# Performance work log

Measured on AMD Instinct MI355X. Metric: run time of the kernel, lower is better.

## Reference

```python
import jax, jax.numpy as jnp
import numpy as np

D = 2048          # in_features == out_features (d_model)
H_TOTAL = 8192    # hidden_features, split across experts
E = 8             # num_experts
K = 2             # num_selects (top-k)
HE = H_TOTAL // E # per-expert hidden size
B, S = 2, 2048


def setup_inputs() -> dict:
    key = jax.random.key(0)
    ks = jax.random.split(key, 8)
    scale_up = 1.0 / np.sqrt(D)
    scale_dn = 1.0 / np.sqrt(HE)
    return {
        "x": jax.random.normal(ks[0], (B, S, D), dtype=jnp.float32),
        # mlp gate network: Linear(D,E,no bias) -> tanh -> Linear(E,E,no bias)
        "Wg1": jax.random.normal(ks[1], (E, D), dtype=jnp.float32) * 0.02,
        "Wg2": jax.random.normal(ks[2], (E, E), dtype=jnp.float32) * 0.2,
        # per-expert GLU-MLP weights (stacked over expert axis)
        "Wup": jax.random.uniform(ks[3], (E, HE, D), dtype=jnp.float32, minval=-scale_up, maxval=scale_up),
        "bup": jax.random.uniform(ks[4], (E, HE), dtype=jnp.float32, minval=-scale_up, maxval=scale_up),
        "Wdown": jax.random.uniform(ks[5], (E, D, HE), dtype=jnp.float32, minval=-scale_dn, maxval=scale_dn),
        "bdown": jax.random.uniform(ks[6], (E, D), dtype=jnp.float32, minval=-scale_dn, maxval=scale_dn),
    }


def reference(x, Wg1, Wg2, Wup, bup, Wdown, bdown):
    Bd, Sd, Dd = x.shape
    T = Bd * Sd
    xt = x.reshape(T, Dd)                                   # [T, D] tokens

    # ---- TopKBalancedNoisyGate (eval mode: no noise) ----
    logits = jnp.tanh(xt @ Wg1.T) @ Wg2.T                   # [T, E]
    _, top_idx = jax.lax.top_k(logits, K)                   # [T, K]
    top_logits = jnp.take_along_axis(logits, top_idx, axis=1)
    top_scores = jax.nn.softmax(top_logits.astype(jnp.float32), axis=1).astype(logits.dtype)
    # scatter top-k scores into dense [T, E] (zeros elsewhere)
    rows = jnp.arange(T)[:, None]
    scores = jnp.zeros_like(logits).at[rows, top_idx].set(top_scores)

    # ---- per-expert Linear-GLU experts: up -> silu -> down, score-combined ----
    up = jnp.einsum('td,ehd->teh', xt, Wup) + bup           # [T, E, HE]
    h = jax.nn.silu(up)
    down = jnp.einsum('teh,eoh->teo', h, Wdown) + bdown     # [T, E, D]
    out = jnp.einsum('te,teo->to', scores, down)            # [T, D]
    return out.reshape(Bd, Sd, Dd)
```

## Files before the change

### kernel.cpp

```cpp
#include <hip/hip_runtime.h>
#include <hip/hip_bf16.h>

#define D_DIM 2048
#define HE_DIM 1024
#define E_NUM 8
#define T_NUM 4096
#define TK_NUM 8192
#define TILE 128
#define BK 64
#define MAXROWS 9216
#define MAXMT 72

#define M_CNT(e)  ((e) * 32)
#define M_FILL(e) (256 + (e) * 32)
#define M_OFF  512
#define M_NMT  520
#define M_TE   528
#define M_TB   600
#define M_TICKET 704
#define M_INTS 1024

typedef unsigned short u16;
typedef __attribute__((ext_vector_type(8))) short bf16x8;
typedef __attribute__((ext_vector_type(4))) float f32x4;

#define OFF_XB   ((size_t)0)
#define OFF_WUPB (OFF_XB + (size_t)T_NUM * D_DIM * 2)
#define OFF_SLOT ((size_t)0)
#define OFF_WDNB (OFF_WUPB + (size_t)E_NUM * HE_DIM * D_DIM * 2)
#define OFF_H    (OFF_WDNB + (size_t)E_NUM * D_DIM * HE_DIM * 2)
#define OFF_SCR  (OFF_H + (size_t)MAXROWS * HE_DIM * 2)
#define OFF_EIDX (OFF_SCR + (size_t)TK_NUM * 4)
#define OFF_RT   (OFF_EIDX + (size_t)TK_NUM * 4)
#define OFF_RS   (OFF_RT + (size_t)MAXROWS * 4)
#define OFF_META (OFF_RS + (size_t)MAXROWS * 4)

__device__ __forceinline__ u16 f2bf(float f) {
  unsigned u = __float_as_uint(f);
  u += 0x7FFFu + ((u >> 16) & 1u);
  return (u16)(u >> 16);
}
__device__ __forceinline__ float bf_lo(unsigned u) { return __uint_as_float(u << 16); }
__device__ __forceinline__ float bf_hi(unsigned u) { return __uint_as_float(u & 0xFFFF0000u); }

__device__ __forceinline__ void gload16(const void* g, void* l) {
  __builtin_amdgcn_global_load_lds((const __attribute__((address_space(1))) void*)g,
                                   (__attribute__((address_space(3))) void*)l,
                                   16, 0, 0);
}

__global__ void k_cvt2(const float4* __restrict__ s1, const float4* __restrict__ s2,
                       ushort4* __restrict__ d1, ushort4* __restrict__ d2, int n4,
                       int* __restrict__ meta, int* __restrict__ rows_slot,
                       float* __restrict__ rowscore) {
  const int i0 = blockIdx.x * blockDim.x + threadIdx.x;
  if (i0 < M_INTS) meta[i0] = 0;
  if (i0 < MAXROWS) { rows_slot[i0] = -1; rowscore[i0] = 0.0f; }
  const int st = gridDim.x * blockDim.x;
  for (int i = i0; i < 2 * n4; i += st) {
    const float4* s = (i < n4) ? s1 : s2;
    ushort4* d = (i < n4) ? d1 : d2;
    int j = (i < n4) ? i : i - n4;
    float4 v = s[j];
    ushort4 o;
    o.x = f2bf(v.x); o.y = f2bf(v.y); o.z = f2bf(v.z); o.w = f2bf(v.w);
    d[j] = o;
  }
}

__global__ __launch_bounds__(256) void k_gate(
    const float4* __restrict__ x4, const float4* __restrict__ Wg1_4,
    const float* __restrict__ Wg2, ushort4* __restrict__ xb4,
    int* __restrict__ eidx, float* __restrict__ scr, int* __restrict__ meta) {
  __shared__ float4 wg1s[E_NUM * (D_DIM / 4)];
  __shared__ int cnt_s[E_NUM];
  __shared__ int lastf;
  const int tid = threadIdx.x;
  if (tid < E_NUM) cnt_s[tid] = 0;
#pragma unroll
  for (int i = 0; i < 16; ++i) wg1s[tid + i * 256] = Wg1_4[tid + i * 256];
  __syncthreads();

  const int w = tid >> 6;
  const int lane = tid & 63;
  for (int j = 0; j < 4; ++j) {
    const int t = blockIdx.x * 16 + w * 4 + j;
    float acc[E_NUM];
#pragma unroll
    for (int e = 0; e < E_NUM; ++e) acc[e] = 0.f;
#pragma unroll
    for (int i = 0; i < 8; ++i) {
      const int c = lane + i * 64;
      float4 xv = x4[(size_t)t * 512 + c];
      ushort4 o;
      o.x = f2bf(xv.x); o.y = f2bf(xv.y); o.z = f2bf(xv.z); o.w = f2bf(xv.w);
      xb4[(size_t)t * 512 + c] = o;
#pragma unroll
      for (int e = 0; e < E_NUM; ++e) {
        float4 wv = wg1s[e * 512 + c];
        acc[e] += xv.x * wv.x + xv.y * wv.y + xv.z * wv.z + xv.w * wv.w;
      }
    }
#pragma unroll
    for (int e = 0; e < E_NUM; ++e) {
      float v = acc[e];
#pragma unroll
      for (int off = 32; off; off >>= 1) v += __shfl_xor(v, off, 64);
      acc[e] = v;
    }
    if (lane == 0) {
      float l1[E_NUM], lg[E_NUM];
#pragma unroll
      for (int e = 0; e < E_NUM; ++e) l1[e] = tanhf(acc[e]);
#pragma unroll
      for (int i = 0; i < E_NUM; ++i) {
        float s = 0.f;
#pragma unroll
        for (int e = 0; e < E_NUM; ++e) s += l1[e] * Wg2[i * E_NUM + e];
        lg[i] = s;
      }
      int i0 = 0; float v0 = lg[0];
#pragma unroll
      for (int i = 1; i < E_NUM; ++i) if (lg[i] > v0) { v0 = lg[i]; i0 = i; }
      int i1 = -1; float v1 = -3.4e38f;
#pragma unroll
      for (int i = 0; i < E_NUM; ++i) if (i != i0 && lg[i] > v1) { v1 = lg[i]; i1 = i; }
      float e1 = __expf(v1 - v0);
      float s0 = 1.f / (1.f + e1);
      float s1 = e1 * s0;
      eidx[t * 2] = i0; eidx[t * 2 + 1] = i1;
      scr[t * 2] = s0;  scr[t * 2 + 1] = s1;
      atomicAdd(&cnt_s[i0], 1);
      atomicAdd(&cnt_s[i1], 1);
    }
  }
  __syncthreads();
  if (tid < E_NUM) atomicAdd(&meta[M_CNT(tid)], cnt_s[tid]);

  if (tid == 0) {
    __threadfence();
    lastf = (atomicAdd(&meta[M_TICKET], 1) == (int)gridDim.x - 1);
  }
  __syncthreads();
  if (lastf && tid < 64) {
    const int l2 = tid;
    int cnt = (l2 < E_NUM) ? atomicAdd(&meta[M_CNT(l2)], 0) : 0;
    int tiles = (cnt + TILE - 1) / TILE;
    int pre = tiles;
#pragma unroll
    for (int off = 1; off < E_NUM; off <<= 1) {
      int v = __shfl_up(pre, off, 64);
      if (l2 >= off && l2 < E_NUM) pre += v;
    }
    int tb_excl = pre - tiles;
    if (l2 < E_NUM) meta[M_OFF + l2] = tb_excl * TILE;
    const int nmt = __shfl(pre, E_NUM - 1, 64);
    if (l2 == 0) meta[M_NMT] = nmt;
    int tb[E_NUM];
#pragma unroll
    for (int k = 0; k < E_NUM; ++k) tb[k] = __shfl(tb_excl, k, 64);
    for (int mt = l2; mt < nmt; mt += 64) {
      int e = 0;
#pragma unroll
      for (int k = 1; k < E_NUM; ++k) if (mt >= tb[k]) e = k;
      meta[M_TE + mt] = e;
      meta[M_TB + mt] = mt * TILE;
    }
  }
}

__global__ void k_assign(const int* __restrict__ eidx, const float* __restrict__ scr,
                         int* __restrict__ meta, int* __restrict__ rows_slot,
                         float* __restrict__ rowscore) {
  int i = blockIdx.x * blockDim.x + threadIdx.x;
  const int lane = threadIdx.x & 63;
  int e = eidx[i];
  int pos = 0;
#pragma unroll
  for (int ex = 0; ex < E_NUM; ++ex) {
    unsigned long long m = __ballot(e == ex);
    if (e == ex) {
      int leader = __ffsll((long long)m) - 1;
      int rank = __popcll(m & ((1ull << lane) - 1ull));
      int b = 0;
      if (lane == leader) b = atomicAdd(&meta[M_FILL(ex)], __popcll(m));
      b = __shfl(b, leader, 64);
      pos = b + rank;
    }
  }
  int r = meta[M_OFF + e] + pos;
  rows_slot[r] = i;
  rowscore[r] = scr[i];
}

__global__ __launch_bounds__(512) void k_up(
    const u16* __restrict__ xb, const u16* __restrict__ wupb,
    const float* __restrict__ bup, const int* __restrict__ meta,
    const int* __restrict__ rows_slot, u16* __restrict__ hbuf) {
  const int mt = blockIdx.y;
  if (mt >= meta[M_NMT]) return;
  const int e = meta[M_TE + mt];
  const int mbase = meta[M_TB + mt];
  const int nt = blockIdx.x;

  __shared__ u16 As[2][TILE * BK];
  __shared__ u16 Bs[2][TILE * BK];

  const int tid = threadIdx.x;
  const int lane = tid & 63;
  const int w = tid >> 6;
  const int r0 = tid >> 3;
  const int cb = (((tid & 7) ^ (r0 & 7)) * 8);

  const u16* gA[2];
  const u16* gB[2];
#pragma unroll
  for (int j = 0; j < 2; ++j) {
    int s = rows_slot[mbase + r0 + 64 * j]; if (s < 0) s = 0;
    gA[j] = xb + (size_t)(s >> 1) * D_DIM + cb;
    gB[j] = wupb + ((size_t)e * HE_DIM + nt * TILE + r0 + 64 * j) * D_DIM + cb;
  }

  const int wm = (w & 1) * 64;
  const int wn = (w >> 1) * 32;
  const int quad = lane >> 4;
  const int l16 = lane & 15;
  const int sw = l16 & 7;

  f32x4 acc[4][2] = {};

#define STAGE_UP(buf, k0) \
  { gload16(gA[0] + (k0), &As[buf][tid * 8]);        \
    gload16(gA[1] + (k0), &As[buf][tid * 8 + 4096]); \
    gload16(gB[0] + (k0), &Bs[buf][tid * 8]);        \
    gload16(gB[1] + (k0), &Bs[buf][tid * 8 + 4096]); }

  STAGE_UP(0, 0);
  __syncthreads();
  int cur = 0;
  for (int k0 = 0; k0 < D_DIM; k0 += BK) {
    if (k0 + BK < D_DIM) STAGE_UP(cur ^ 1, k0 + BK);
    const u16* pa0 = &As[cur][(wm + l16) * BK];
    const u16* pb0 = &Bs[cur][(wn + l16) * BK];
#pragma unroll
    for (int h = 0; h < 2; ++h) {
      const int off = ((h * 4 + quad) ^ sw) * 8;
      bf16x8 af[4], bfr[2];
#pragma unroll
      for (int i = 0; i < 4; ++i) af[i] = *(const bf16x8*)(pa0 + i * 16 * BK + off);
#pragma unroll
      for (int i = 0; i < 2; ++i) bfr[i] = *(const bf16x8*)(pb0 + i * 16 * BK + off);
#pragma unroll
      for (int mi = 0; mi < 4; ++mi)
#pragma unroll
        for (int ni = 0; ni < 2; ++ni)
          acc[mi][ni] = __builtin_amdgcn_mfma_f32_16x16x32_bf16(af[mi], bfr[ni], acc[mi][ni], 0, 0, 0);
    }
    __syncthreads();
    cur ^= 1;
  }

#pragma unroll
  for (int mi = 0; mi < 4; ++mi) {
    const int m = wm + mi * 16 + quad * 4;
#pragma unroll
    for (int ni = 0; ni < 2; ++ni) {
      const int ng = nt * TILE + wn + ni * 16 + l16;
      const float bias = bup[e * HE_DIM + ng];
#pragma unroll
      for (int r = 0; r < 4; ++r) {
        float v = acc[mi][ni][r] + bias;
        v = v / (1.0f + __expf(-v));
        hbuf[(size_t)(mbase + m + r) * HE_DIM + ng] = f2bf(v);
      }
    }
  }
}

__global__ __launch_bounds__(512) void k_down(
    const u16* __restrict__ hbuf, const u16* __restrict__ wdnb,
    const float* __restrict__ bdown, const int* __restrict__ meta,
    const int* __restrict__ rows_slot, const float* __restrict__ rowscore,
    u16* __restrict__ slot) {
  const int mt = blockIdx.y;
  if (mt >= meta[M_NMT]) return;
  const int e = meta[M_TE + mt];
  const int mbase = meta[M_TB + mt];
  const int nt = blockIdx.x;

  __shared__ u16 As[2][TILE * BK];
  __shared__ u16 Bs[2][TILE * BK];

  const int tid = threadIdx.x;
  const int lane = tid & 63;
  const int w = tid >> 6;
  const int r0 = tid >> 3;
  const int cb = (((tid & 7) ^ (r0 & 7)) * 8);

  const u16* gA[2];
  const u16* gB[2];
#pragma unroll
  for (int j = 0; j < 2; ++j) {
    gA[j] = hbuf + (size_t)(mbase + r0 + 64 * j) * HE_DIM + cb;
    gB[j] = wdnb + ((size_t)e * D_DIM + nt * TILE + r0 + 64 * j) * HE_DIM + cb;
  }

  const int wm = (w & 1) * 64;
  const int wn = (w >> 1) * 32;
  const int quad = lane >> 4;
  const int l16 = lane & 15;
  const int sw = l16 & 7;

  f32x4 acc[4][2] = {};

#define STAGE_DN(buf, k0) \
  { gload16(gA[0] + (k0), &As[buf][tid * 8]);        \
    gload16(gA[1] + (k0), &As[buf][tid * 8 + 4096]); \
    gload16(gB[0] + (k0), &Bs[buf][tid * 8]);        \
    gload16(gB[1] + (k0), &Bs[buf][tid * 8 + 4096]); }

  STAGE_DN(0, 0);
  __syncthreads();
  int cur = 0;
  for (int k0 = 0; k0 < HE_DIM; k0 += BK) {
    if (k0 + BK < HE_DIM) STAGE_DN(cur ^ 1, k0 + BK);
    const u16* pa0 = &As[cur][(wm + l16) * BK];
    const u16* pb0 = &Bs[cur][(wn + l16) * BK];
#pragma unroll
    for (int h = 0; h < 2; ++h) {
      const int off = ((h * 4 + quad) ^ sw) * 8;
      bf16x8 af[4], bfr[2];
#pragma unroll
      for (int i = 0; i < 4; ++i) af[i] = *(const bf16x8*)(pa0 + i * 16 * BK + off);
#pragma unroll
      for (int i = 0; i < 2; ++i) bfr[i] = *(const bf16x8*)(pb0 + i * 16 * BK + off);
#pragma unroll
      for (int mi = 0; mi < 4; ++mi)
#pragma unroll
        for (int ni = 0; ni < 2; ++ni)
          acc[mi][ni] = __builtin_amdgcn_mfma_f32_16x16x32_bf16(af[mi], bfr[ni], acc[mi][ni], 0, 0, 0);
    }
    __syncthreads();
    cur ^= 1;
  }

#pragma unroll
  for (int mi = 0; mi < 4; ++mi) {
    const int m = wm + mi * 16 + quad * 4;
#pragma unroll
    for (int r = 0; r < 4; ++r) {
      const int rg = mbase + m + r;
      const int s = rows_slot[rg];
      const float sc = rowscore[rg];
      if (s < 0) continue;
      u16* dst = slot + (size_t)s * D_DIM;
#pragma unroll
      for (int ni = 0; ni < 2; ++ni) {
        const int ng = nt * TILE + wn + ni * 16 + l16;
        float v = (acc[mi][ni][r] + bdown[e * D_DIM + ng]) * sc;
        dst[ng] = f2bf(v);
      }
    }
  }
}

__global__ __launch_bounds__(256) void k_combine(const u16* __restrict__ slot,
                                                 float* __restrict__ out) {
  int i = blockIdx.x * blockDim.x + threadIdx.x;
  int t = i >> 8;
  int c = i & 255;
  const uint4* p0 = (const uint4*)(slot + (size_t)(t * 2) * D_DIM) + c;
  const uint4* p1 = (const uint4*)(slot + (size_t)(t * 2 + 1) * D_DIM) + c;
  uint4 a = *p0, b = *p1;
  float4 o0, o1;
  o0.x = bf_lo(a.x) + bf_lo(b.x);  o0.y = bf_hi(a.x) + bf_hi(b.x);
  o0.z = bf_lo(a.y) + bf_lo(b.y);  o0.w = bf_hi(a.y) + bf_hi(b.y);
  o1.x = bf_lo(a.z) + bf_lo(b.z);  o1.y = bf_hi(a.z) + bf_hi(b.z);
  o1.z = bf_lo(a.w) + bf_lo(b.w);  o1.w = bf_hi(a.w) + bf_hi(b.w);
  float4* po = (float4*)(out + (size_t)t * D_DIM) + c * 2;
  po[0] = o0;
  po[1] = o1;
}

extern "C" void kernel_launch(void* const* d_in, const int* in_sizes, int n_in,
                              void* d_out, int out_size, void* d_ws, size_t ws_size,
                              hipStream_t stream) {
  const float* x     = (const float*)d_in[0];
  const float* Wg1   = (const float*)d_in[1];
  const float* Wg2   = (const float*)d_in[2];
  const float* Wup   = (const float*)d_in[3];
  const float* bup   = (const float*)d_in[4];
  const float* Wdown = (const float*)d_in[5];
  const float* bdown = (const float*)d_in[6];
  float* out = (float*)d_out;

  char* ws = (char*)d_ws;
  u16*   xb         = (u16*)(ws + OFF_XB);
  u16*   wupb       = (u16*)(ws + OFF_WUPB);
  u16*   wdnb       = (u16*)(ws + OFF_WDNB);
  u16*   hbuf       = (u16*)(ws + OFF_H);
  u16*   slotbuf    = (u16*)(ws + OFF_SLOT);
  float* scr        = (float*)(ws + OFF_SCR);
  int*   eidx       = (int*)(ws + OFF_EIDX);
  int*   rows_slot  = (int*)(ws + OFF_RT);
  float* rowscore   = (float*)(ws + OFF_RS);
  int*   meta       = (int*)(ws + OFF_META);

  k_cvt2<<<8192, 256, 0, stream>>>((const float4*)Wup, (const float4*)Wdown,
                                   (ushort4*)wupb, (ushort4*)wdnb,
                                   E_NUM * HE_DIM * D_DIM / 4,
                                   meta, rows_slot, rowscore);
  k_gate<<<T_NUM / 16, 256, 0, stream>>>((const float4*)x, (const float4*)Wg1, Wg2,
                                         (ushort4*)xb, eidx, scr, meta);
  k_assign<<<TK_NUM / 256, 256, 0, stream>>>(eidx, scr, meta, rows_slot, rowscore);
  k_up<<<dim3(HE_DIM / TILE, MAXMT), 512, 0, stream>>>(xb, wupb, bup, meta, rows_slot, hbuf);
  k_down<<<dim3(D_DIM / TILE, MAXMT), 512, 0, stream>>>(hbuf, wdnb, bdown, meta,
                                                        rows_slot, rowscore, slotbuf);
  k_combine<<<T_NUM * D_DIM / 8 / 256, 256, 0, stream>>>(slotbuf, out);
}
```

Before: 365.7 us.

## Triple-buffer LDS staging with partial vmcnt waits in expert GEMMs

Both the up and down expert GEMM kernels move from double to triple-buffered LDS tiles, prefetching two k-steps ahead. The full __syncthreads drain is replaced with s_waitcnt vmcnt(4) plus a raw barrier, so the next tile's global-to-LDS loads stay in flight across the barrier. The goal is to hide global load latency behind MFMA work. In exchange, LDS use per block rises from 64KB to 96KB, which can cut occupancy, and correctness depends on the hand-counted vmcnt matching the four loads issued per stage.

```diff
diff --git a/kernel.cpp b/kernel.cpp
--- a/kernel.cpp
+++ b/kernel.cpp
@@ -48,6 +48,10 @@
                                    (__attribute__((address_space(3))) void*)l,
                                    16, 0, 0);
 }
+
+#define WAIT_VM4 asm volatile("s_waitcnt vmcnt(4)" ::: "memory")
+#define WAIT_VM0 asm volatile("s_waitcnt vmcnt(0)" ::: "memory")
+#define SBAR     { __builtin_amdgcn_s_barrier(); asm volatile("" ::: "memory"); }
 
 __global__ void k_cvt2(const float4* __restrict__ s1, const float4* __restrict__ s2,
                        ushort4* __restrict__ d1, ushort4* __restrict__ d2, int n4,
@@ -203,8 +207,8 @@
   const int mbase = meta[M_TB + mt];
   const int nt = blockIdx.x;
 
-  __shared__ u16 As[2][TILE * BK];
-  __shared__ u16 Bs[2][TILE * BK];
+  __shared__ u16 As[3][TILE * BK];
+  __shared__ u16 Bs[3][TILE * BK];
 
   const int tid = threadIdx.x;
   const int lane = tid & 63;
@@ -236,10 +240,13 @@
     gload16(gB[1] + (k0), &Bs[buf][tid * 8 + 4096]); }
 
   STAGE_UP(0, 0);
-  __syncthreads();
-  int cur = 0;
+  STAGE_UP(1, BK);
+  WAIT_VM4;
+  SBAR;
+  int cur = 0, nxt = 2;
   for (int k0 = 0; k0 < D_DIM; k0 += BK) {
-    if (k0 + BK < D_DIM) STAGE_UP(cur ^ 1, k0 + BK);
+    const bool pf = (k0 + 2 * BK < D_DIM);
+    if (pf) STAGE_UP(nxt, k0 + 2 * BK);
     const u16* pa0 = &As[cur][(wm + l16) * BK];
     const u16* pb0 = &Bs[cur][(wn + l16) * BK];
 #pragma unroll
@@ -256,8 +263,10 @@
         for (int ni = 0; ni < 2; ++ni)
           acc[mi][ni] = __builtin_amdgcn_mfma_f32_16x16x32_bf16(af[mi], bfr[ni], acc[mi][ni], 0, 0, 0);
     }
-    __syncthreads();
-    cur ^= 1;
+    if (pf) { WAIT_VM4; } else { WAIT_VM0; }
+    SBAR;
+    cur = (cur == 2) ? 0 : cur + 1;
+    nxt = (nxt == 2) ? 0 : nxt + 1;
   }
 
 #pragma unroll
@@ -288,8 +297,8 @@
   const int mbase = meta[M_TB + mt];
   const int nt = blockIdx.x;
 
-  __shared__ u16 As[2][TILE * BK];
-  __shared__ u16 Bs[2][TILE * BK];
+  __shared__ u16 As[3][TILE * BK];
+  __shared__ u16 Bs[3][TILE * BK];
 
   const int tid = threadIdx.x;
   const int lane = tid & 63;
@@ -320,10 +329,13 @@
     gload16(gB[1] + (k0), &Bs[buf][tid * 8 + 4096]); }
 
   STAGE_DN(0, 0);
-  __syncthreads();
-  int cur = 0;
+  STAGE_DN(1, BK);
+  WAIT_VM4;
+  SBAR;
+  int cur = 0, nxt = 2;
   for (int k0 = 0; k0 < HE_DIM; k0 += BK) {
-    if (k0 + BK < HE_DIM) STAGE_DN(cur ^ 1, k0 + BK);
+    const bool pf = (k0 + 2 * BK < HE_DIM);
+    if (pf) STAGE_DN(nxt, k0 + 2 * BK);
     const u16* pa0 = &As[cur][(wm + l16) * BK];
     const u16* pb0 = &Bs[cur][(wn + l16) * BK];
 #pragma unroll
@@ -340,8 +352,10 @@
         for (int ni = 0; ni < 2; ++ni)
           acc[mi][ni] = __builtin_amdgcn_mfma_f32_16x16x32_bf16(af[mi], bfr[ni], acc[mi][ni], 0, 0, 0);
     }
-    __syncthreads();
-    cur ^= 1;
+    if (pf) { WAIT_VM4; } else { WAIT_VM0; }
+    SBAR;
+    cur = (cur == 2) ? 0 : cur + 1;
+    nxt = (nxt == 2) ? 0 : nxt + 1;
   }
 
 #pragma unroll
```

New measurement: 420.7 us. 1.15x slower.

## Fuse fp32-to-bf16 weight conversion into expert GEMM tile loads

Applied to the files above, without the earlier changes.

Drops the separate pass that converted all expert up and down weights to bf16 in workspace. The GEMM kernels now read fp32 weights straight into registers, convert them to bf16, and write them to shared memory after the MFMA work for the current tile, so the loads overlap compute. This removes a large read-and-write pass over the weights. In exchange, each weight tile is re-read in fp32 (twice the bytes) by every M-tile block, and conversion work is repeated across blocks and adds register pressure.

```diff
diff --git a/kernel.cpp b/kernel.cpp
--- a/kernel.cpp
+++ b/kernel.cpp
@@ -25,10 +25,8 @@
 typedef __attribute__((ext_vector_type(4))) float f32x4;
 
 #define OFF_XB   ((size_t)0)
-#define OFF_WUPB (OFF_XB + (size_t)T_NUM * D_DIM * 2)
 #define OFF_SLOT ((size_t)0)
-#define OFF_WDNB (OFF_WUPB + (size_t)E_NUM * HE_DIM * D_DIM * 2)
-#define OFF_H    (OFF_WDNB + (size_t)E_NUM * D_DIM * HE_DIM * 2)
+#define OFF_H    ((size_t)33554432)
 #define OFF_SCR  (OFF_H + (size_t)MAXROWS * HE_DIM * 2)
 #define OFF_EIDX (OFF_SCR + (size_t)TK_NUM * 4)
 #define OFF_RT   (OFF_EIDX + (size_t)TK_NUM * 4)
@@ -49,23 +47,11 @@
                                    16, 0, 0);
 }
 
-__global__ void k_cvt2(const float4* __restrict__ s1, const float4* __restrict__ s2,
-                       ushort4* __restrict__ d1, ushort4* __restrict__ d2, int n4,
-                       int* __restrict__ meta, int* __restrict__ rows_slot,
+__global__ void k_init(int* __restrict__ meta, int* __restrict__ rows_slot,
                        float* __restrict__ rowscore) {
-  const int i0 = blockIdx.x * blockDim.x + threadIdx.x;
-  if (i0 < M_INTS) meta[i0] = 0;
-  if (i0 < MAXROWS) { rows_slot[i0] = -1; rowscore[i0] = 0.0f; }
-  const int st = gridDim.x * blockDim.x;
-  for (int i = i0; i < 2 * n4; i += st) {
-    const float4* s = (i < n4) ? s1 : s2;
-    ushort4* d = (i < n4) ? d1 : d2;
-    int j = (i < n4) ? i : i - n4;
-    float4 v = s[j];
-    ushort4 o;
-    o.x = f2bf(v.x); o.y = f2bf(v.y); o.z = f2bf(v.z); o.w = f2bf(v.w);
-    d[j] = o;
-  }
+  int i = blockIdx.x * blockDim.x + threadIdx.x;
+  if (i < M_INTS) meta[i] = 0;
+  if (i < MAXROWS) { rows_slot[i] = -1; rowscore[i] = 0.0f; }
 }
 
 __global__ __launch_bounds__(256) void k_gate(
@@ -194,7 +180,7 @@
 }
 
 __global__ __launch_bounds__(512) void k_up(
-    const u16* __restrict__ xb, const u16* __restrict__ wupb,
+    const u16* __restrict__ xb, const float* __restrict__ Wup,
     const float* __restrict__ bup, const int* __restrict__ meta,
     const int* __restrict__ rows_slot, u16* __restrict__ hbuf) {
   const int mt = blockIdx.y;
@@ -213,12 +199,12 @@
   const int cb = (((tid & 7) ^ (r0 & 7)) * 8);
 
   const u16* gA[2];
-  const u16* gB[2];
+  const float* gB[2];
 #pragma unroll
   for (int j = 0; j < 2; ++j) {
     int s = rows_slot[mbase + r0 + 64 * j]; if (s < 0) s = 0;
     gA[j] = xb + (size_t)(s >> 1) * D_DIM + cb;
-    gB[j] = wupb + ((size_t)e * HE_DIM + nt * TILE + r0 + 64 * j) * D_DIM + cb;
+    gB[j] = Wup + ((size_t)e * HE_DIM + nt * TILE + r0 + 64 * j) * D_DIM + cb;
   }
 
   const int wm = (w & 1) * 64;
@@ -228,18 +214,34 @@
   const int sw = l16 & 7;
 
   f32x4 acc[4][2] = {};
-
-#define STAGE_UP(buf, k0) \
-  { gload16(gA[0] + (k0), &As[buf][tid * 8]);        \
-    gload16(gA[1] + (k0), &As[buf][tid * 8 + 4096]); \
-    gload16(gB[0] + (k0), &Bs[buf][tid * 8]);        \
-    gload16(gB[1] + (k0), &Bs[buf][tid * 8 + 4096]); }
-
-  STAGE_UP(0, 0);
+  float4 br[2][2];
+
+#define A_STAGE_UP(buf, k0) \
+  { gload16(gA[0] + (k0), &As[buf][tid * 8]); \
+    gload16(gA[1] + (k0), &As[buf][tid * 8 + 4096]); }
+#define B_LOAD_UP(k0) \
+  { br[0][0] = *(const float4*)(gB[0] + (k0)); \
+    br[0][1] = *(const float4*)(gB[0] + (k0) + 4); \
+    br[1][0] = *(const float4*)(gB[1] + (k0)); \
+    br[1][1] = *(const float4*)(gB[1] + (k0) + 4); }
+#define B_WRITE_UP(buf) \
+  { _Pragma("unroll") \
+    for (int j = 0; j < 2; ++j) { \
+      bf16x8 v; \
+      v[0] = (short)f2bf(br[j][0].x); v[1] = (short)f2bf(br[j][0].y); \
+      v[2] = (short)f2bf(br[j][0].z); v[3] = (short)f2bf(br[j][0].w); \
+      v[4] = (short)f2bf(br[j][1].x); v[5] = (short)f2bf(br[j][1].y); \
+      v[6] = (short)f2bf(br[j][1].z); v[7] = (short)f2bf(br[j][1].w); \
+      *(bf16x8*)(&Bs[buf][tid * 8 + 4096 * j]) = v; } }
+
+  B_LOAD_UP(0);
+  A_STAGE_UP(0, 0);
+  B_WRITE_UP(0);
   __syncthreads();
   int cur = 0;
   for (int k0 = 0; k0 < D_DIM; k0 += BK) {
-    if (k0 + BK < D_DIM) STAGE_UP(cur ^ 1, k0 + BK);
+    const bool pf = (k0 + BK < D_DIM);
+    if (pf) { B_LOAD_UP(k0 + BK); A_STAGE_UP(cur ^ 1, k0 + BK); }
     const u16* pa0 = &As[cur][(wm + l16) * BK];
     const u16* pb0 = &Bs[cur][(wn + l16) * BK];
 #pragma unroll
@@ -256,6 +258,7 @@
         for (int ni = 0; ni < 2; ++ni)
           acc[mi][ni] = __builtin_amdgcn_mfma_f32_16x16x32_bf16(af[mi], bfr[ni], acc[mi][ni], 0, 0, 0);
     }
+    if (pf) B_WRITE_UP(cur ^ 1);
     __syncthreads();
     cur ^= 1;
   }
@@ -278,7 +281,7 @@
 }
 
 __global__ __launch_bounds__(512) void k_down(
-    const u16* __restrict__ hbuf, const u16* __restrict__ wdnb,
+    const u16* __restrict__ hbuf, const float* __restrict__ Wdown,
     const float* __restrict__ bdown, const int* __restrict__ meta,
     const int* __restrict__ rows_slot, const float* __restrict__ rowscore,
     u16* __restrict__ slot) {
@@ -298,11 +301,11 @@
   const int cb = (((tid & 7) ^ (r0 & 7)) * 8);
 
   const u16* gA[2];
-  const u16* gB[2];
+  const float* gB[2];
 #pragma unroll
   for (int j = 0; j < 2; ++j) {
     gA[j] = hbuf + (size_t)(mbase + r0 + 64 * j) * HE_DIM + cb;
-    gB[j] = wdnb + ((size_t)e * D_DIM + nt * TILE + r0 + 64 * j) * HE_DIM + cb;
+    gB[j] = Wdown + ((size_t)e * D_DIM + nt * TILE + r0 + 64 * j) * HE_DIM + cb;
   }
 
   const int wm = (w & 1) * 64;
@@ -312,18 +315,34 @@
   const int sw = l16 & 7;
 
   f32x4 acc[4][2] = {};
-
-#define STAGE_DN(buf, k0) \
-  { gload16(gA[0] + (k0), &As[buf][tid * 8]);        \
-    gload16(gA[1] + (k0), &As[buf][tid * 8 + 4096]); \
-    gload16(gB[0] + (k0), &Bs[buf][tid * 8]);        \
-    gload16(gB[1] + (k0), &Bs[buf][tid * 8 + 4096]); }
-
-  STAGE_DN(0, 0);
+  float4 br[2][2];
+
+#define A_STAGE_DN(buf, k0) \
+  { gload16(gA[0] + (k0), &As[buf][tid * 8]); \
+    gload16(gA[1] + (k0), &As[buf][tid * 8 + 4096]); }
+#define B_LOAD_DN(k0) \
+  { br[0][0] = *(const float4*)(gB[0] + (k0)); \
+    br[0][1] = *(const float4*)(gB[0] + (k0) + 4); \
+    br[1][0] = *(const float4*)(gB[1] + (k0)); \
+    br[1][1] = *(const float4*)(gB[1] + (k0) + 4); }
+#define B_WRITE_DN(buf) \
+  { _Pragma("unroll") \
+    for (int j = 0; j < 2; ++j) { \
+      bf16x8 v; \
+      v[0] = (short)f2bf(br[j][0].x); v[1] = (short)f2bf(br[j][0].y); \
+      v[2] = (short)f2bf(br[j][0].z); v[3] = (short)f2bf(br[j][0].w); \
+      v[4] = (short)f2bf(br[j][1].x); v[5] = (short)f2bf(br[j][1].y); \
+      v[6] = (short)f2bf(br[j][1].z); v[7] = (short)f2bf(br[j][1].w); \
+      *(bf16x8*)(&Bs[buf][tid * 8 + 4096 * j]) = v; } }
+
+  B_LOAD_DN(0);
+  A_STAGE_DN(0, 0);
+  B_WRITE_DN(0);
   __syncthreads();
   int cur = 0;
   for (int k0 = 0; k0 < HE_DIM; k0 += BK) {
-    if (k0 + BK < HE_DIM) STAGE_DN(cur ^ 1, k0 + BK);
+    const bool pf = (k0 + BK < HE_DIM);
+    if (pf) { B_LOAD_DN(k0 + BK); A_STAGE_DN(cur ^ 1, k0 + BK); }
     const u16* pa0 = &As[cur][(wm + l16) * BK];
     const u16* pb0 = &Bs[cur][(wn + l16) * BK];
 #pragma unroll
@@ -340,6 +359,7 @@
         for (int ni = 0; ni < 2; ++ni)
           acc[mi][ni] = __builtin_amdgcn_mfma_f32_16x16x32_bf16(af[mi], bfr[ni], acc[mi][ni], 0, 0, 0);
     }
+    if (pf) B_WRITE_DN(cur ^ 1);
     __syncthreads();
     cur ^= 1;
   }
@@ -396,8 +416,6 @@
 
   char* ws = (char*)d_ws;
   u16*   xb         = (u16*)(ws + OFF_XB);
-  u16*   wupb       = (u16*)(ws + OFF_WUPB);
-  u16*   wdnb       = (u16*)(ws + OFF_WDNB);
   u16*   hbuf       = (u16*)(ws + OFF_H);
   u16*   slotbuf    = (u16*)(ws + OFF_SLOT);
   float* scr        = (float*)(ws + OFF_SCR);
@@ -406,15 +424,12 @@
   float* rowscore   = (float*)(ws + OFF_RS);
   int*   meta       = (int*)(ws + OFF_META);
 
-  k_cvt2<<<8192, 256, 0, stream>>>((const float4*)Wup, (const float4*)Wdown,
-                                   (ushort4*)wupb, (ushort4*)wdnb,
-                                   E_NUM * HE_DIM * D_DIM / 4,
-                                   meta, rows_slot, rowscore);
+  k_init<<<(MAXROWS + 255) / 256, 256, 0, stream>>>(meta, rows_slot, rowscore);
   k_gate<<<T_NUM / 16, 256, 0, stream>>>((const float4*)x, (const float4*)Wg1, Wg2,
                                          (ushort4*)xb, eidx, scr, meta);
   k_assign<<<TK_NUM / 256, 256, 0, stream>>>(eidx, scr, meta, rows_slot, rowscore);
-  k_up<<<dim3(HE_DIM / TILE, MAXMT), 512, 0, stream>>>(xb, wupb, bup, meta, rows_slot, hbuf);
-  k_down<<<dim3(D_DIM / TILE, MAXMT), 512, 0, stream>>>(hbuf, wdnb, bdown, meta,
+  k_up<<<dim3(HE_DIM / TILE, MAXMT), 512, 0, stream>>>(xb, Wup, bup, meta, rows_slot, hbuf);
+  k_down<<<dim3(D_DIM / TILE, MAXMT), 512, 0, stream>>>(hbuf, Wdown, bdown, meta,
                                                         rows_slot, rowscore, slotbuf);
   k_combine<<<T_NUM * D_DIM / 8 / 256, 256, 0, stream>>>(slotbuf, out);
 }
```

After: 392.5 us. 1.07x slower.
